# Kernel tuning notes

Measured on AMD Instinct MI355X. Metric: run time of the kernel, lower is better.

Reference implementation:

```python
import jax, jax.numpy as jnp
import numpy as np

N_HEADS = 8
LN_EPS = 1e-5


def _layernorm(x, g, b):
    mu = jnp.mean(x, axis=-1, keepdims=True)
    var = jnp.var(x, axis=-1, keepdims=True)
    return (x - mu) * jax.lax.rsqrt(var + LN_EPS) * g + b


def _mha(xq, xkv, W, bvec):
    # W: [4, D, D] stacked (Wq, Wk, Wv, Wo); bvec: [4, D]
    Wq, Wk, Wv, Wo = W[0], W[1], W[2], W[3]
    bq, bk, bv, bo = bvec[0], bvec[1], bvec[2], bvec[3]
    B, Lq, D = xq.shape
    Lk = xkv.shape[1]
    dh = D // N_HEADS
    q = (xq @ Wq + bq).reshape(B, Lq, N_HEADS, dh)
    k = (xkv @ Wk + bk).reshape(B, Lk, N_HEADS, dh)
    v = (xkv @ Wv + bv).reshape(B, Lk, N_HEADS, dh)
    scores = jnp.einsum('bqhd,bkhd->bhqk', q, k) / jnp.sqrt(jnp.asarray(dh, xq.dtype))
    attn = jax.nn.softmax(scores, axis=-1)
    out = jnp.einsum('bhqk,bkhd->bqhd', attn, v).reshape(B, Lq, D)
    return out @ Wo + bo


def setup_inputs() -> dict:
    key = jax.random.key(0)
    ks = jax.random.split(key, 8)
    B, A, D, F = 64, 512, 256, 512
    s = 0.02
    return {
        'trg': jax.random.normal(ks[0], (B, A, D), jnp.float32),
        'src': jax.random.normal(ks[1], (B, A, D), jnp.float32),
        'W_sa': jax.random.normal(ks[2], (4, D, D), jnp.float32) * s,
        'b_sa': jnp.zeros((4, D), jnp.float32),
        'W_ea': jax.random.normal(ks[3], (4, D, D), jnp.float32) * s,
        'b_ea': jnp.zeros((4, D), jnp.float32),
        'ln_g': jnp.ones((D,), jnp.float32),
        'ln_b': jnp.zeros((D,), jnp.float32),
        'W_fc1': jax.random.normal(ks[4], (D, F), jnp.float32) * s,
        'b_fc1': jnp.zeros((F,), jnp.float32),
        'W_fc2': jax.random.normal(ks[5], (F, F), jnp.float32) * s,
        'b_fc2': jnp.zeros((F,), jnp.float32),
        'W_out': jax.random.normal(ks[6], (F, 2), jnp.float32) * s,
        'b_out': jnp.zeros((2,), jnp.float32),
    }


def reference(trg, src, W_sa, b_sa, W_ea, b_ea, ln_g, ln_b,
              W_fc1, b_fc1, W_fc2, b_fc2, W_out, b_out):
    # n_layers = 1 decoder layer: self-attn + cross-attn, residual + LayerNorm
    h = _layernorm(trg + _mha(trg, trg, W_sa, b_sa), ln_g, ln_b)
    h = _layernorm(h + _mha(h, src, W_ea, b_ea), ln_g, ln_b)
    # norm+softmax weighted-sum pooling (fused replacement of the double loop)
    atom_norm = jnp.linalg.norm(h, axis=2)            # [B, A]
    w = jax.nn.softmax(atom_norm, axis=1)             # [B, A]
    pooled = jnp.einsum('ba,bad->bd', w, h)           # [B, D]
    # fc stack (dropout is identity in eval mode)
    h1 = jax.nn.relu(pooled @ W_fc1 + b_fc1)
    h2 = jax.nn.relu(h1 @ W_fc2 + b_fc2)
    return h2 @ W_out + b_out                          # [B, 2]
```

## Files before the change

kernel.cpp:

```cpp
#include <hip/hip_runtime.h>

typedef unsigned short u16;
typedef __attribute__((ext_vector_type(8))) short s16x8;
typedef __attribute__((ext_vector_type(8))) _Float16 f16x8;
typedef __attribute__((ext_vector_type(4))) float f32x4;

#define ASYNC16(gp, lp) \
  __builtin_amdgcn_global_load_lds((__attribute__((address_space(1))) void*)(gp), \
                                   (__attribute__((address_space(3))) void*)(lp), 16, 0, 0)

__device__ __forceinline__ u16 f2h(float f) {
  _Float16 h = (_Float16)f;
  union { _Float16 h; u16 u; } v; v.h = h;
  return v.u;
}
__device__ __forceinline__ float h2f(u16 s) {
  union { _Float16 h; u16 u; } v; v.u = s; return (float)v.h;
}

__device__ __forceinline__ int swz4(int row) { return (row & 3) ^ ((row >> 2) & 3); }

__global__ __launch_bounds__(256) void prep_kernel(
    const float* __restrict__ trg, const float* __restrict__ src,
    const float* __restrict__ Wsa, const float* __restrict__ Wea,
    u16* __restrict__ trg_h, u16* __restrict__ src_h, u16* __restrict__ wt)
{
  int blk = blockIdx.x, tid = threadIdx.x;
  if (blk < 8192) {
    const float* sp = (blk < 4096) ? trg : src;
    u16* dp = (blk < 4096) ? trg_h : src_h;
    size_t base = ((size_t)(blk & 4095) * 256 + tid) * 8;
    float4 a = *(const float4*)(sp + base);
    float4 c = *(const float4*)(sp + base + 4);
    s16x8 o;
    o[0] = (short)f2h(a.x); o[1] = (short)f2h(a.y);
    o[2] = (short)f2h(a.z); o[3] = (short)f2h(a.w);
    o[4] = (short)f2h(c.x); o[5] = (short)f2h(c.y);
    o[6] = (short)f2h(c.z); o[7] = (short)f2h(c.w);
    *(s16x8*)(dp + base) = o;
  } else {
    int t = (blk - 8192) * 256 + tid;
    int row = t >> 8, k = t & 255;
    const float* W; int sel, col;
    if (row < 768)       { W = Wsa; sel = row >> 8;              col = row & 255; }
    else if (row < 1024) { W = Wsa; sel = 3;                     col = row & 255; }
    else if (row < 1280) { W = Wea; sel = 0;                     col = row & 255; }
    else if (row < 1792) { W = Wea; sel = ((row - 1280) >> 8) + 1; col = (row - 1280) & 255; }
    else                 { W = Wea; sel = 3;                     col = row & 255; }
    wt[(size_t)row * 256 + k] = f2h(W[sel * 65536 + k * 256 + col]);
  }
}

__global__ __launch_bounds__(256, 3) void gemm_bias_f16(
    const u16* __restrict__ A, const u16* __restrict__ Bt,
    const float* __restrict__ bias, u16* __restrict__ C, int N)
{
  __shared__ u16 Asm[128 * 32];
  __shared__ u16 Bsm[128 * 32];
  const int tid = threadIdx.x;
  const int wv = tid >> 6, ln = tid & 63;
  const int quad = ln >> 4, l16 = ln & 15;
  const int nblk = blockIdx.x;
  const size_t arow0 = (size_t)blockIdx.y * 128;
  const size_t brow0 = (size_t)nblk * 128;
  const int wr = wv >> 1, wc = wv & 1;
  f32x4 acc[4][4];
  const f32x4 VZERO = {0.f, 0.f, 0.f, 0.f};
#pragma unroll
  for (int i = 0; i < 4; ++i)
#pragma unroll
    for (int j = 0; j < 4; ++j) acc[i][j] = VZERO;

  for (int k0 = 0; k0 < 256; k0 += 32) {
    __syncthreads();
#pragma unroll
    for (int j = 0; j < 2; ++j) {
      int c = (j * 4 + wv) * 64 + ln;
      int row = c >> 2, slot = c & 3;
      int kc = slot ^ swz4(row);
      ASYNC16(A + (arow0 + row) * 256 + k0 + kc * 8, Asm + c * 8);
      ASYNC16(Bt + (brow0 + row) * 256 + k0 + kc * 8, Bsm + c * 8);
    }
    __syncthreads();
    f16x8 af[4], bfr[4];
#pragma unroll
    for (int mt = 0; mt < 4; ++mt) {
      int tr = wr * 64 + mt * 16 + l16;
      int slot = quad ^ swz4(tr);
      af[mt] = *(const f16x8*)(Asm + (tr * 4 + slot) * 8);
    }
#pragma unroll
    for (int nt = 0; nt < 4; ++nt) {
      int tr = wc * 64 + nt * 16 + l16;
      int slot = quad ^ swz4(tr);
      bfr[nt] = *(const f16x8*)(Bsm + (tr * 4 + slot) * 8);
    }
#pragma unroll
    for (int mt = 0; mt < 4; ++mt)
#pragma unroll
      for (int nt = 0; nt < 4; ++nt)
        acc[mt][nt] = __builtin_amdgcn_mfma_f32_16x16x32_f16(af[mt], bfr[nt], acc[mt][nt], 0, 0, 0);
  }
#pragma unroll
  for (int nt = 0; nt < 4; ++nt) {
    int col = nblk * 128 + wc * 64 + nt * 16 + l16;
    float bz = bias[col];
#pragma unroll
    for (int mt = 0; mt < 4; ++mt) {
      size_t row0 = arow0 + wr * 64 + mt * 16 + quad * 4;
#pragma unroll
      for (int r = 0; r < 4; ++r)
        C[(row0 + r) * (size_t)N + col] = f2h(acc[mt][nt][r] + bz);
    }
  }
}

__global__ __launch_bounds__(256, 3) void attn_mfma(
    const u16* __restrict__ Qp, int ldq,
    const u16* __restrict__ Kp, int ldk,
    const u16* __restrict__ Vp, int ldv,
    u16* __restrict__ Op)
{
  __shared__ u16 Ks[256 * 40];
  __shared__ u16 Vt[32 * 264];
  __shared__ __align__(16) unsigned Pw[4][32 * 20];
  const int tid = threadIdx.x;
  const int wv = tid >> 6, ln = tid & 63;
  const int quad = ln >> 4, l16 = ln & 15;
  const int lin = blockIdx.x;
  const int qb = (lin >> 3) & 3;
  const int g = ((lin >> 5) << 3) | (lin & 7);
  const int h = g & 7;
  const size_t rb = (size_t)(g >> 3) * 512;
  const f32x4 VZERO = {0.f, 0.f, 0.f, 0.f};

  f16x8 qf[2];
  const _Float16 qs = (_Float16)0.25503492f;
#pragma unroll
  for (int mq = 0; mq < 2; ++mq) {
    int qrow = qb * 128 + wv * 32 + mq * 16 + l16;
    qf[mq] = *(const f16x8*)(Qp + (rb + qrow) * (size_t)ldq + h * 32 + quad * 8);
#pragma unroll
    for (int j = 0; j < 8; ++j) qf[mq][j] *= qs;
  }
  f16x8 onesf;
#pragma unroll
  for (int j = 0; j < 8; ++j) onesf[j] = (_Float16)1.0f;

  f32x4 o[2][2], osum[2];
#pragma unroll
  for (int mq = 0; mq < 2; ++mq) { o[mq][0] = VZERO; o[mq][1] = VZERO; osum[mq] = VZERO; }

  for (int kb = 0; kb < 2; ++kb) {
    __syncthreads();
    for (int c = tid; c < 1024; c += 256) {
      int row = c >> 2, part = c & 3;
      s16x8 kv = *(const s16x8*)(Kp + (rb + kb * 256 + row) * (size_t)ldk + h * 32 + part * 8);
      *(s16x8*)(Ks + row * 40 + part * 8) = kv;
      s16x8 vv = *(const s16x8*)(Vp + (rb + kb * 256 + row) * (size_t)ldv + h * 32 + part * 8);
      int kts = row >> 5, l = row & 31;
      int p = 2 * (l & 15) + (l >> 4);
#pragma unroll
      for (int j = 0; j < 8; ++j) Vt[(part * 8 + j) * 264 + kts * 32 + p] = (u16)vv[j];
    }
    __syncthreads();
    for (int kt = 0; kt < 8; ++kt) {
      f16x8 kf0 = *(const f16x8*)(Ks + (kt * 32 + l16) * 40 + quad * 8);
      f16x8 kf1 = *(const f16x8*)(Ks + (kt * 32 + 16 + l16) * 40 + quad * 8);
      f16x8 vf0 = *(const f16x8*)(Vt + l16 * 264 + kt * 32 + quad * 8);
      f16x8 vf1 = *(const f16x8*)(Vt + (16 + l16) * 264 + kt * 32 + quad * 8);
#pragma unroll
      for (int mq = 0; mq < 2; ++mq) {
        f32x4 s0 = __builtin_amdgcn_mfma_f32_16x16x32_f16(qf[mq], kf0, VZERO, 0, 0, 0);
        f32x4 s1 = __builtin_amdgcn_mfma_f32_16x16x32_f16(qf[mq], kf1, VZERO, 0, 0, 0);
#pragma unroll
        for (int r = 0; r < 4; ++r) {
          float e0 = __builtin_amdgcn_exp2f(s0[r]);
          float e1 = __builtin_amdgcn_exp2f(s1[r]);
          union { _Float16 h2[2]; unsigned u; } pk;
          pk.h2[0] = (_Float16)e0; pk.h2[1] = (_Float16)e1;
          Pw[wv][(mq * 16 + quad * 4 + r) * 20 + l16] = pk.u;
        }
      }
#pragma unroll
      for (int mq = 0; mq < 2; ++mq) {
        f16x8 pf = *(const f16x8*)(&Pw[wv][(mq * 16 + l16) * 20 + quad * 4]);
        o[mq][0] = __builtin_amdgcn_mfma_f32_16x16x32_f16(pf, vf0, o[mq][0], 0, 0, 0);
        o[mq][1] = __builtin_amdgcn_mfma_f32_16x16x32_f16(pf, vf1, o[mq][1], 0, 0, 0);
        osum[mq] = __builtin_amdgcn_mfma_f32_16x16x32_f16(pf, onesf, osum[mq], 0, 0, 0);
      }
    }
  }
#pragma unroll
  for (int mq = 0; mq < 2; ++mq)
#pragma unroll
    for (int r = 0; r < 4; ++r) {
      float inv = 1.f / osum[mq][r];
      size_t row = rb + qb * 128 + wv * 32 + mq * 16 + quad * 4 + r;
      Op[row * 256 + h * 32 + l16]      = f2h(o[mq][0][r] * inv);
      Op[row * 256 + h * 32 + 16 + l16] = f2h(o[mq][1][r] * inv);
    }
}

__global__ __launch_bounds__(256, 3) void lnproj_kernel(
    const u16* __restrict__ A, const u16* __restrict__ Wt,
    const float* __restrict__ bo, const u16* __restrict__ resid,
    const float* __restrict__ g, const float* __restrict__ lb,
    u16* __restrict__ Hh, float* __restrict__ norms)
{
  __shared__ u16 Asm[64 * 32];
  __shared__ u16 Bsm[256 * 32];
  const int tid = threadIdx.x;
  const int wv = tid >> 6, ln = tid & 63;
  const int quad = ln >> 4, l16 = ln & 15;
  const size_t arow0 = (size_t)blockIdx.x * 64;
  f32x4 acc[16];
  const f32x4 VZERO = {0.f, 0.f, 0.f, 0.f};
#pragma unroll
  for (int nt = 0; nt < 16; ++nt) acc[nt] = VZERO;

  for (int k0 = 0; k0 < 256; k0 += 32) {
    __syncthreads();
    {
      int c = tid;
      int row = c >> 2, slot = c & 3;
      int kc = slot ^ swz4(row);
      ASYNC16(A + (arow0 + row) * 256 + k0 + kc * 8, Asm + c * 8);
    }
#pragma unroll
    for (int j = 0; j < 4; ++j) {
      int c = (j * 4 + wv) * 64 + ln;
      int row = c >> 2, slot = c & 3;
      int kc = slot ^ swz4(row);
      ASYNC16(Wt + (size_t)row * 256 + k0 + kc * 8, Bsm + c * 8);
    }
    __syncthreads();
    int tr = wv * 16 + l16;
    int aslot = quad ^ swz4(tr);
    f16x8 af = *(const f16x8*)(Asm + (tr * 4 + aslot) * 8);
#pragma unroll
    for (int nt = 0; nt < 16; ++nt) {
      int br = nt * 16 + l16;
      int bslot = quad ^ swz4(br);
      f16x8 bfr = *(const f16x8*)(Bsm + (br * 4 + bslot) * 8);
      acc[nt] = __builtin_amdgcn_mfma_f32_16x16x32_f16(af, bfr, acc[nt], 0, 0, 0);
    }
  }
  float gv[16], bv[16], bov[16];
#pragma unroll
  for (int nt = 0; nt < 16; ++nt) {
    int col = nt * 16 + l16;
    gv[nt] = g[col]; bv[nt] = lb[col]; bov[nt] = bo[col];
  }
#pragma unroll
  for (int r = 0; r < 4; ++r) {
    size_t row = arow0 + wv * 16 + quad * 4 + r;
    const u16* rrow = resid + row * 256;
    float vals[16]; float s = 0.f;
#pragma unroll
    for (int nt = 0; nt < 16; ++nt) {
      float v = acc[nt][r] + bov[nt] + h2f(rrow[nt * 16 + l16]);
      vals[nt] = v; s += v;
    }
#pragma unroll
    for (int m = 1; m < 16; m <<= 1) s += __shfl_xor(s, m);
    float mean = s * (1.f / 256.f);
    float sq = 0.f;
#pragma unroll
    for (int nt = 0; nt < 16; ++nt) { float d = vals[nt] - mean; sq = fmaf(d, d, sq); }
#pragma unroll
    for (int m = 1; m < 16; m <<= 1) sq += __shfl_xor(sq, m);
    float rstd = rsqrtf(sq * (1.f / 256.f) + 1e-5f);
    float ssq = 0.f;
#pragma unroll
    for (int nt = 0; nt < 16; ++nt) {
      float hv = (vals[nt] - mean) * rstd * gv[nt] + bv[nt];
      Hh[row * 256 + nt * 16 + l16] = f2h(hv);
      ssq = fmaf(hv, hv, ssq);
    }
    if (norms) {
#pragma unroll
      for (int m = 1; m < 16; m <<= 1) ssq += __shfl_xor(ssq, m);
      if (l16 == 0) norms[row] = sqrtf(ssq);
    }
  }
}

__global__ __launch_bounds__(256) void softmax_kernel(const float* norms, float* w,
                                                      float* __restrict__ pooled)
{
  int b = blockIdx.x, tid = threadIdx.x;
  int ln = tid & 63, wvi = tid >> 6;
  __shared__ float red[8];
  const float* nb = norms + b * 512;
  float n0 = nb[tid], n1 = nb[tid + 256];
  float mx = fmaxf(n0, n1);
#pragma unroll
  for (int m = 1; m < 64; m <<= 1) mx = fmaxf(mx, __shfl_xor(mx, m));
  if (ln == 0) red[wvi] = mx;
  __syncthreads();
  mx = fmaxf(fmaxf(red[0], red[1]), fmaxf(red[2], red[3]));
  float e0 = __expf(n0 - mx), e1 = __expf(n1 - mx);
  float s = e0 + e1;
#pragma unroll
  for (int m = 1; m < 64; m <<= 1) s += __shfl_xor(s, m);
  if (ln == 0) red[4 + wvi] = s;
  __syncthreads();
  s = red[4] + red[5] + red[6] + red[7];
  float inv = 1.f / s;
  w[b * 512 + tid] = e0 * inv;
  w[b * 512 + tid + 256] = e1 * inv;
  pooled[b * 256 + tid] = 0.f;
}

__global__ __launch_bounds__(256) void poolsum_kernel(const float* __restrict__ w,
                                                      const u16* __restrict__ h,
                                                      float* __restrict__ pooled)
{
  int b = blockIdx.x, sl = blockIdx.y, d = threadIdx.x;
  const u16* hb = h + ((size_t)b * 512 + sl * 64) * 256 + d;
  const float* wb = w + b * 512 + sl * 64;
  float acc = 0.f;
#pragma unroll 8
  for (int a = 0; a < 64; ++a) acc = fmaf(wb[a], h2f(hb[(size_t)a * 256]), acc);
  atomicAdd(&pooled[b * 256 + d], acc);
}

__global__ __launch_bounds__(512) void fc1_kernel(
    const float* __restrict__ pooled, const float* __restrict__ Wfc1,
    const float* __restrict__ bfc1, float* __restrict__ x1)
{
  int b = blockIdx.x, tid = threadIdx.x;
  __shared__ float px[256];
  if (tid < 256) px[tid] = pooled[b * 256 + tid];
  __syncthreads();
  float a = bfc1[tid];
#pragma unroll 8
  for (int d = 0; d < 256; ++d) a = fmaf(px[d], Wfc1[d * 512 + tid], a);
  x1[b * 512 + tid] = fmaxf(a, 0.f);
}

__global__ __launch_bounds__(512) void fc23_kernel(
    const float* __restrict__ x1, const float* __restrict__ Wfc2,
    const float* __restrict__ bfc2, const float* __restrict__ Wout,
    const float* __restrict__ bout, float* __restrict__ out)
{
  int b = blockIdx.x, tid = threadIdx.x;
  __shared__ float sx[512];
  __shared__ float rr[16];
  sx[tid] = x1[b * 512 + tid];
  __syncthreads();
  float a = bfc2[tid];
#pragma unroll 8
  for (int d = 0; d < 512; ++d) a = fmaf(sx[d], Wfc2[d * 512 + tid], a);
  a = fmaxf(a, 0.f);
  float p0 = a * Wout[tid * 2];
  float p1 = a * Wout[tid * 2 + 1];
  int ln = tid & 63, wvi = tid >> 6;
#pragma unroll
  for (int m = 1; m < 64; m <<= 1) { p0 += __shfl_xor(p0, m); p1 += __shfl_xor(p1, m); }
  if (ln == 0) { rr[wvi] = p0; rr[8 + wvi] = p1; }
  __syncthreads();
  if (tid == 0) {
    float s = 0.f;
#pragma unroll
    for (int i = 0; i < 8; ++i) s += rr[i];
    out[b * 2] = s + bout[0];
  }
  if (tid == 1) {
    float s = 0.f;
#pragma unroll
    for (int i = 0; i < 8; ++i) s += rr[8 + i];
    out[b * 2 + 1] = s + bout[1];
  }
}

extern "C" void kernel_launch(void* const* d_in, const int* in_sizes, int n_in,
                              void* d_out, int out_size, void* d_ws, size_t ws_size,
                              hipStream_t stream) {
  const float* trg  = (const float*)d_in[0];
  const float* src  = (const float*)d_in[1];
  const float* Wsa  = (const float*)d_in[2];
  const float* bsa  = (const float*)d_in[3];
  const float* Wea  = (const float*)d_in[4];
  const float* bea  = (const float*)d_in[5];
  const float* lng  = (const float*)d_in[6];
  const float* lnb  = (const float*)d_in[7];
  const float* Wfc1 = (const float*)d_in[8];
  const float* bfc1 = (const float*)d_in[9];
  const float* Wfc2 = (const float*)d_in[10];
  const float* bfc2 = (const float*)d_in[11];
  const float* Wout = (const float*)d_in[12];
  const float* bout = (const float*)d_in[13];
  float* out = (float*)d_out;

  const size_t M = 32768;
  char* ws = (char*)d_ws;
  u16* trg_h = (u16*)ws;                ws += M * 256 * 2;
  u16* src_h = (u16*)ws;                ws += M * 256 * 2;
  u16* wt     = (u16*)ws;               ws += 2048 * 256 * 2;
  u16* qkv    = (u16*)ws;               ws += M * 768 * 2;
  u16* attnb  = (u16*)ws;               ws += M * 256 * 2;
  u16* hh     = (u16*)ws;               ws += M * 256 * 2;
  u16* h2h    = (u16*)ws;               ws += M * 256 * 2;
  float* norms = (float*)ws;            ws += M * 4;
  float* pooled = (float*)ws;           ws += 64 * 256 * 4;
  float* x1buf = (float*)ws;            ws += 64 * 512 * 4;

  u16* wt_sa_qkv = wt;
  u16* wt_sa_o   = wt + 768 * 256;
  u16* wt_ea_q   = wt + 1024 * 256;
  u16* wt_ea_kv  = wt + 1280 * 256;
  u16* wt_ea_o   = wt + 1792 * 256;
  u16* kvb = qkv + M * 256;

  prep_kernel<<<10240, 256, 0, stream>>>(trg, src, Wsa, Wea, trg_h, src_h, wt);
  gemm_bias_f16<<<dim3(6, 256), 256, 0, stream>>>(trg_h, wt_sa_qkv, bsa, qkv, 768);
  attn_mfma<<<2048, 256, 0, stream>>>(qkv, 768, qkv + 256, 768, qkv + 512, 768, attnb);
  lnproj_kernel<<<512, 256, 0, stream>>>(attnb, wt_sa_o, bsa + 768, trg_h, lng, lnb,
                                         hh, nullptr);
  gemm_bias_f16<<<dim3(2, 256), 256, 0, stream>>>(hh, wt_ea_q, bea, qkv, 256);
  gemm_bias_f16<<<dim3(4, 256), 256, 0, stream>>>(src_h, wt_ea_kv, bea + 256, kvb, 512);
  attn_mfma<<<2048, 256, 0, stream>>>(qkv, 256, kvb, 512, kvb + 256, 512, attnb);
  lnproj_kernel<<<512, 256, 0, stream>>>(attnb, wt_ea_o, bea + 768, hh, lng, lnb,
                                         h2h, norms);
  softmax_kernel<<<64, 256, 0, stream>>>(norms, norms, pooled);
  poolsum_kernel<<<dim3(64, 8), 256, 0, stream>>>(norms, h2h, pooled);
  fc1_kernel<<<64, 512, 0, stream>>>(pooled, Wfc1, bfc1, x1buf);
  fc23_kernel<<<64, 512, 0, stream>>>(x1buf, Wfc2, bfc2, Wout, bout, out);

  (void)in_sizes; (void)n_in; (void)out_size; (void)ws_size;
}
```

Before: 339.1 us.

## Merge QKV and cross-KV GEMMs, tile weight transpose, fuse FC layers

Runs the self-attention QKV projection and the cross-attention KV projection of src in a single dual GEMM launch, giving kvb its own buffer. Replaces the scalar, uncoalesced weight transpose in prep with an LDS-tiled transpose, and moves zeroing of pooled into prep. Fuses fc1 and fc2/out into one kernel. These changes cut launches and uncoalesced weight reads and fill the GPU better on the dual GEMM, at the cost of extra workspace and 8192 prep blocks that allocate an unused 36KB LDS array, which may lower occupancy for the conversion blocks.

```diff
diff --git a/kernel.cpp b/kernel.cpp
--- a/kernel.cpp
+++ b/kernel.cpp
@@ -23,8 +23,10 @@
 __global__ __launch_bounds__(256) void prep_kernel(
     const float* __restrict__ trg, const float* __restrict__ src,
     const float* __restrict__ Wsa, const float* __restrict__ Wea,
-    u16* __restrict__ trg_h, u16* __restrict__ src_h, u16* __restrict__ wt)
-{
+    u16* __restrict__ trg_h, u16* __restrict__ src_h, u16* __restrict__ wt,
+    float* __restrict__ pooled)
+{
+  __shared__ __align__(16) u16 T[256 * 72];
   int blk = blockIdx.x, tid = threadIdx.x;
   if (blk < 8192) {
     const float* sp = (blk < 4096) ? trg : src;
@@ -38,29 +40,44 @@
     o[4] = (short)f2h(c.x); o[5] = (short)f2h(c.y);
     o[6] = (short)f2h(c.z); o[7] = (short)f2h(c.w);
     *(s16x8*)(dp + base) = o;
+  } else if (blk < 8224) {
+    int t = blk - 8192;
+    int m = t >> 2, k0 = (t & 3) * 64;
+    const float* W = (m < 4) ? (Wsa + m * 65536) : (Wea + (m - 4) * 65536);
+#pragma unroll
+    for (int pass = 0; pass < 16; ++pass) {
+      int r = pass * 4 + (tid >> 6);
+      int c4 = (tid & 63) * 4;
+      float4 v = *(const float4*)(W + (size_t)(k0 + r) * 256 + c4);
+      T[(c4 + 0) * 72 + r] = f2h(v.x);
+      T[(c4 + 1) * 72 + r] = f2h(v.y);
+      T[(c4 + 2) * 72 + r] = f2h(v.z);
+      T[(c4 + 3) * 72 + r] = f2h(v.w);
+    }
+    __syncthreads();
+#pragma unroll
+    for (int pass = 0; pass < 4; ++pass) {
+      int n = pass * 64 + (tid >> 2);
+      int koff = (tid & 3) * 16;
+      s16x8 a = *(const s16x8*)(T + n * 72 + koff);
+      s16x8 b = *(const s16x8*)(T + n * 72 + koff + 8);
+      u16* dst = wt + (size_t)(m * 256 + n) * 256 + k0 + koff;
+      *(s16x8*)dst = a;
+      *(s16x8*)(dst + 8) = b;
+    }
   } else {
-    int t = (blk - 8192) * 256 + tid;
-    int row = t >> 8, k = t & 255;
-    const float* W; int sel, col;
-    if (row < 768)       { W = Wsa; sel = row >> 8;              col = row & 255; }
-    else if (row < 1024) { W = Wsa; sel = 3;                     col = row & 255; }
-    else if (row < 1280) { W = Wea; sel = 0;                     col = row & 255; }
-    else if (row < 1792) { W = Wea; sel = ((row - 1280) >> 8) + 1; col = (row - 1280) & 255; }
-    else                 { W = Wea; sel = 3;                     col = row & 255; }
-    wt[(size_t)row * 256 + k] = f2h(W[sel * 65536 + k * 256 + col]);
-  }
-}
-
-__global__ __launch_bounds__(256, 3) void gemm_bias_f16(
+    pooled[(blk - 8224) * 256 + tid] = 0.f;
+  }
+}
+
+__device__ __forceinline__ void gemm_body(
     const u16* __restrict__ A, const u16* __restrict__ Bt,
-    const float* __restrict__ bias, u16* __restrict__ C, int N)
-{
-  __shared__ u16 Asm[128 * 32];
-  __shared__ u16 Bsm[128 * 32];
+    const float* __restrict__ bias, u16* __restrict__ C, int N, int nblk,
+    u16* Asm, u16* Bsm)
+{
   const int tid = threadIdx.x;
   const int wv = tid >> 6, ln = tid & 63;
   const int quad = ln >> 4, l16 = ln & 15;
-  const int nblk = blockIdx.x;
   const size_t arow0 = (size_t)blockIdx.y * 128;
   const size_t brow0 = (size_t)nblk * 128;
   const int wr = wv >> 1, wc = wv & 1;
@@ -113,6 +130,29 @@
         C[(row0 + r) * (size_t)N + col] = f2h(acc[mt][nt][r] + bz);
     }
   }
+}
+
+__global__ __launch_bounds__(256, 3) void gemm_bias_f16(
+    const u16* __restrict__ A, const u16* __restrict__ Bt,
+    const float* __restrict__ bias, u16* __restrict__ C, int N)
+{
+  __shared__ u16 Asm[128 * 32];
+  __shared__ u16 Bsm[128 * 32];
+  gemm_body(A, Bt, bias, C, N, blockIdx.x, Asm, Bsm);
+}
+
+__global__ __launch_bounds__(256, 3) void gemm_dual(
+    const u16* __restrict__ A0, const u16* __restrict__ Bt0,
+    const float* __restrict__ bias0, u16* __restrict__ C0, int N0, int nx0,
+    const u16* __restrict__ A1, const u16* __restrict__ Bt1,
+    const float* __restrict__ bias1, u16* __restrict__ C1, int N1)
+{
+  __shared__ u16 Asm[128 * 32];
+  __shared__ u16 Bsm[128 * 32];
+  if ((int)blockIdx.x < nx0)
+    gemm_body(A0, Bt0, bias0, C0, N0, blockIdx.x, Asm, Bsm);
+  else
+    gemm_body(A1, Bt1, bias1, C1, N1, blockIdx.x - nx0, Asm, Bsm);
 }
 
 __global__ __launch_bounds__(256, 3) void attn_mfma(
@@ -286,8 +326,7 @@
   }
 }
 
-__global__ __launch_bounds__(256) void softmax_kernel(const float* norms, float* w,
-                                                      float* __restrict__ pooled)
+__global__ __launch_bounds__(256) void softmax_kernel(const float* norms, float* w)
 {
   int b = blockIdx.x, tid = threadIdx.x;
   int ln = tid & 63, wvi = tid >> 6;
@@ -310,7 +349,6 @@
   float inv = 1.f / s;
   w[b * 512 + tid] = e0 * inv;
   w[b * 512 + tid + 256] = e1 * inv;
-  pooled[b * 256 + tid] = 0.f;
 }
 
 __global__ __launch_bounds__(256) void poolsum_kernel(const float* __restrict__ w,
@@ -326,33 +364,25 @@
   atomicAdd(&pooled[b * 256 + d], acc);
 }
 
-__global__ __launch_bounds__(512) void fc1_kernel(
-    const float* __restrict__ pooled, const float* __restrict__ Wfc1,
-    const float* __restrict__ bfc1, float* __restrict__ x1)
+__global__ __launch_bounds__(512) void fc_fused(
+    const float* __restrict__ pooled,
+    const float* __restrict__ Wfc1, const float* __restrict__ bfc1,
+    const float* __restrict__ Wfc2, const float* __restrict__ bfc2,
+    const float* __restrict__ Wout, const float* __restrict__ bout,
+    float* __restrict__ out)
 {
   int b = blockIdx.x, tid = threadIdx.x;
-  __shared__ float px[256];
+  __shared__ float px[256], x1[512], rr[16];
   if (tid < 256) px[tid] = pooled[b * 256 + tid];
   __syncthreads();
   float a = bfc1[tid];
 #pragma unroll 8
   for (int d = 0; d < 256; ++d) a = fmaf(px[d], Wfc1[d * 512 + tid], a);
-  x1[b * 512 + tid] = fmaxf(a, 0.f);
-}
-
-__global__ __launch_bounds__(512) void fc23_kernel(
-    const float* __restrict__ x1, const float* __restrict__ Wfc2,
-    const float* __restrict__ bfc2, const float* __restrict__ Wout,
-    const float* __restrict__ bout, float* __restrict__ out)
-{
-  int b = blockIdx.x, tid = threadIdx.x;
-  __shared__ float sx[512];
-  __shared__ float rr[16];
-  sx[tid] = x1[b * 512 + tid];
+  x1[tid] = fmaxf(a, 0.f);
   __syncthreads();
-  float a = bfc2[tid];
+  a = bfc2[tid];
 #pragma unroll 8
-  for (int d = 0; d < 512; ++d) a = fmaf(sx[d], Wfc2[d * 512 + tid], a);
+  for (int d = 0; d < 512; ++d) a = fmaf(x1[d], Wfc2[d * 512 + tid], a);
   a = fmaxf(a, 0.f);
   float p0 = a * Wout[tid * 2];
   float p1 = a * Wout[tid * 2 + 1];
@@ -400,34 +430,33 @@
   u16* src_h = (u16*)ws;                ws += M * 256 * 2;
   u16* wt     = (u16*)ws;               ws += 2048 * 256 * 2;
   u16* qkv    = (u16*)ws;               ws += M * 768 * 2;
+  u16* kvb    = (u16*)ws;               ws += M * 512 * 2;
   u16* attnb  = (u16*)ws;               ws += M * 256 * 2;
   u16* hh     = (u16*)ws;               ws += M * 256 * 2;
   u16* h2h    = (u16*)ws;               ws += M * 256 * 2;
   float* norms = (float*)ws;            ws += M * 4;
   float* pooled = (float*)ws;           ws += 64 * 256 * 4;
-  float* x1buf = (float*)ws;            ws += 64 * 512 * 4;
 
   u16* wt_sa_qkv = wt;
   u16* wt_sa_o   = wt + 768 * 256;
   u16* wt_ea_q   = wt + 1024 * 256;
   u16* wt_ea_kv  = wt + 1280 * 256;
   u16* wt_ea_o   = wt + 1792 * 256;
-  u16* kvb = qkv + M * 256;
-
-  prep_kernel<<<10240, 256, 0, stream>>>(trg, src, Wsa, Wea, trg_h, src_h, wt);
-  gemm_bias_f16<<<dim3(6, 256), 256, 0, stream>>>(trg_h, wt_sa_qkv, bsa, qkv, 768);
+
+  prep_kernel<<<8288, 256, 0, stream>>>(trg, src, Wsa, Wea, trg_h, src_h, wt, pooled);
+  gemm_dual<<<dim3(10, 256), 256, 0, stream>>>(
+      trg_h, wt_sa_qkv, bsa, qkv, 768, 6,
+      src_h, wt_ea_kv, bea + 256, kvb, 512);
   attn_mfma<<<2048, 256, 0, stream>>>(qkv, 768, qkv + 256, 768, qkv + 512, 768, attnb);
   lnproj_kernel<<<512, 256, 0, stream>>>(attnb, wt_sa_o, bsa + 768, trg_h, lng, lnb,
                                          hh, nullptr);
   gemm_bias_f16<<<dim3(2, 256), 256, 0, stream>>>(hh, wt_ea_q, bea, qkv, 256);
-  gemm_bias_f16<<<dim3(4, 256), 256, 0, stream>>>(src_h, wt_ea_kv, bea + 256, kvb, 512);
   attn_mfma<<<2048, 256, 0, stream>>>(qkv, 256, kvb, 512, kvb + 256, 512, attnb);
   lnproj_kernel<<<512, 256, 0, stream>>>(attnb, wt_ea_o, bea + 768, hh, lng, lnb,
                                          h2h, norms);
-  softmax_kernel<<<64, 256, 0, stream>>>(norms, norms, pooled);
+  softmax_kernel<<<64, 256, 0, stream>>>(norms, norms);
   poolsum_kernel<<<dim3(64, 8), 256, 0, stream>>>(norms, h2h, pooled);
-  fc1_kernel<<<64, 512, 0, stream>>>(pooled, Wfc1, bfc1, x1buf);
-  fc23_kernel<<<64, 512, 0, stream>>>(x1buf, Wfc2, bfc2, Wout, bout, out);
+  fc_fused<<<64, 512, 0, stream>>>(pooled, Wfc1, bfc1, Wfc2, bfc2, Wout, bout, out);
 
   (void)in_sizes; (void)n_in; (void)out_size; (void)ws_size;
 }
```

Result: slower. 357.6 us (+5.5%).
